# Performance work log

Hardware: AMD Instinct MI355X
Metric: run time of the kernel (lower is better)

## Reference

```python
import jax, jax.numpy as jnp
import numpy as np

B, T, E, H = 4, 4096, 1024, 64  # batch, seq_len, embed dim, head_size


def setup_inputs() -> dict:
    key = jax.random.key(0)
    kx, kk, kq, kv = jax.random.split(key, 4)
    x = jax.random.normal(kx, (B, T, E), dtype=jnp.float32)
    # nn.Linear(E, H, bias=False) weight, stored here as [E, H] (x @ W)
    Wk = jax.random.normal(kk, (E, H), dtype=jnp.float32) * 0.02
    Wq = jax.random.normal(kq, (E, H), dtype=jnp.float32) * 0.02
    Wv = jax.random.normal(kv, (E, H), dtype=jnp.float32) * 0.02
    return {"x": x, "Wk": Wk, "Wq": Wq, "Wv": Wv}


def reference(x, Wk, Wq, Wv):
    # single-head scaled dot-product attention (dropout p=0 -> identity)
    k = jnp.einsum("bte,eh->bth", x, Wk)
    q = jnp.einsum("bte,eh->bth", x, Wq)
    v = jnp.einsum("bte,eh->bth", x, Wv)
    scale = jnp.asarray(H, x.dtype) ** -0.5
    wei = jnp.einsum("bqh,bkh->bqk", q, k) * scale  # [B,T,T]
    wei = jax.nn.softmax(wei, axis=-1)
    out = jnp.einsum("bqk,bkh->bqh", wei, v)  # [B,T,H]
    return out
```

## Files before the change

kernel.cpp:

```cpp
#include <hip/hip_runtime.h>
#include <hip/hip_bf16.h>


typedef __attribute__((ext_vector_type(8))) short short8;
typedef __attribute__((ext_vector_type(4))) short short4v;
typedef __attribute__((ext_vector_type(4))) float f32x4;
typedef __attribute__((ext_vector_type(2))) unsigned uint2v;

#define LOG2E 1.44269504f

__device__ inline short f2bf(float f) {
  union { __hip_bfloat16 h; short s; } u; u.h = __float2bfloat16(f); return u.s;
}
__device__ inline unsigned cvt_pk_bf16(float lo, float hi) {
  unsigned r;
  asm("v_cvt_pk_bf16_f32 %0, %1, %2" : "=v"(r) : "v"(lo), "v"(hi));
  return r;
}
__device__ inline void gl_lds16(const short* g, short* l) {
  __builtin_amdgcn_global_load_lds(
      (const __attribute__((address_space(1))) void*)g,
      (__attribute__((address_space(3))) void*)l, 16, 0, 0);
}
__device__ inline float xsum4g(float x) {
  uint2v a = __builtin_amdgcn_permlane32_swap(__float_as_uint(x), __float_as_uint(x), false, false);
  float y = __uint_as_float(a[0]) + __uint_as_float(a[1]);
  uint2v b = __builtin_amdgcn_permlane16_swap(__float_as_uint(y), __float_as_uint(y), false, false);
  return __uint_as_float(b[0]) + __uint_as_float(b[1]);
}

__global__ __launch_bounds__(256) void wtrans_kernel(
    const float* __restrict__ Wk, const float* __restrict__ Wq, const float* __restrict__ Wv,
    short* __restrict__ wT)
{
  const int m3 = blockIdx.y;
  const float* W = (m3 == 0) ? Wk : (m3 == 1) ? Wq : Wv;
  const float sc = (m3 == 1) ? 0.125f * LOG2E : 1.0f;
  int idx = blockIdx.x * 256 + threadIdx.x;
  int k = idx >> 6;
  int n = idx & 63;
  wT[(size_t)m3 * 65536 + n * 1024 + k] = f2bf(W[idx] * sc);
}

__global__ __launch_bounds__(256) void proj_kernel(
    const float* __restrict__ x, const short* __restrict__ wT,
    short* __restrict__ kout, short* __restrict__ qout, short* __restrict__ vTout)
{
  const int m3 = blockIdx.y;
  __shared__ __align__(16) short xl[64][72];
  __shared__ __align__(16) short wl[64][64];

  const int tid  = threadIdx.x;
  const int w    = tid >> 6;
  const int lane = tid & 63;
  const int lr   = lane & 15;
  const int lg   = lane >> 4;
  const int rowbase = blockIdx.x * 64;
  const short* wb = wT + (size_t)m3 * 65536;

  f32x4 acc[4];
#pragma unroll
  for (int j = 0; j < 4; ++j) acc[j] = (f32x4){0.f, 0.f, 0.f, 0.f};

  const int xr = tid >> 4;
  const int xc = (tid & 15) << 2;

  float4 nx[4];
  short8 nw[2];
#pragma unroll
  for (int p = 0; p < 4; ++p)
    nx[p] = *reinterpret_cast<const float4*>(&x[(size_t)(rowbase + xr + p * 16) * 1024 + xc]);
#pragma unroll
  for (int p = 0; p < 2; ++p) {
    int c = p * 256 + tid;
    nw[p] = *reinterpret_cast<const short8*>(&wb[(size_t)(c >> 3) * 1024 + ((c & 7) << 3)]);
  }

  for (int t = 0; t < 16; ++t) {
    if (t > 0) __syncthreads();

#pragma unroll
    for (int p = 0; p < 4; ++p) {
      uint2v pk;
      pk[0] = cvt_pk_bf16(nx[p].x, nx[p].y);
      pk[1] = cvt_pk_bf16(nx[p].z, nx[p].w);
      *reinterpret_cast<uint2v*>(&xl[xr + p * 16][xc]) = pk;
    }
#pragma unroll
    for (int p = 0; p < 2; ++p) {
      int c = p * 256 + tid;
      int n = c >> 3;
      int kk = (c & 7) << 3;
      *reinterpret_cast<short8*>(&wl[n][kk ^ ((n & 7) << 3)]) = nw[p];
    }
    __syncthreads();

    if (t < 15) {
      const int kb = (t + 1) * 64;
#pragma unroll
      for (int p = 0; p < 4; ++p)
        nx[p] = *reinterpret_cast<const float4*>(
            &x[(size_t)(rowbase + xr + p * 16) * 1024 + kb + xc]);
#pragma unroll
      for (int p = 0; p < 2; ++p) {
        int c = p * 256 + tid;
        nw[p] = *reinterpret_cast<const short8*>(
            &wb[(size_t)(c >> 3) * 1024 + kb + ((c & 7) << 3)]);
      }
    }

#pragma unroll
    for (int ks = 0; ks < 2; ++ks) {
      short8 a = *reinterpret_cast<const short8*>(&xl[16 * w + lr][ks * 32 + lg * 8]);
#pragma unroll
      for (int ct = 0; ct < 4; ++ct) {
        short8 b = *reinterpret_cast<const short8*>(
            &wl[16 * ct + lr][(ks * 32 + lg * 8) ^ ((lr & 7) << 3)]);
        acc[ct] = __builtin_amdgcn_mfma_f32_16x16x32_bf16(a, b, acc[ct], 0, 0, 0);
      }
    }
  }

  if (m3 == 2) {
    const int bb   = rowbase >> 12;
    const int tloc = (rowbase & 4095) + 16 * w + 4 * lg;
#pragma unroll
    for (int ct = 0; ct < 4; ++ct) {
      uint2v pk;
      pk[0] = cvt_pk_bf16(acc[ct][0], acc[ct][1]);
      pk[1] = cvt_pk_bf16(acc[ct][2], acc[ct][3]);
      size_t vidx = (size_t)bb * 64 * 4096 + (size_t)(16 * ct + lr) * 4096 + tloc;
      *reinterpret_cast<uint2v*>(&vTout[vidx]) = pk;
    }
  } else {
    short* out = (m3 == 0) ? kout : qout;
#pragma unroll
    for (int ct = 0; ct < 4; ++ct)
#pragma unroll
      for (int j = 0; j < 4; ++j) {
        int grow = rowbase + 16 * w + 4 * lg + j;
        out[(size_t)grow * 64 + 16 * ct + lr] = f2bf(acc[ct][j]);
      }
  }
}

__device__ __forceinline__ void softmax_t(f32x4 s[4], float& l, short8 pf[2]) {
#pragma unroll
  for (int a = 0; a < 4; ++a)
#pragma unroll
    for (int j = 0; j < 4; ++j) s[a][j] = __builtin_amdgcn_exp2f(s[a][j]);
  float ps = ((s[0][0] + s[0][1]) + (s[0][2] + s[0][3]))
           + ((s[1][0] + s[1][1]) + (s[1][2] + s[1][3]))
           + ((s[2][0] + s[2][1]) + (s[2][2] + s[2][3]))
           + ((s[3][0] + s[3][1]) + (s[3][2] + s[3][3]));
  l += ps;

  unsigned u[4][2];
#pragma unroll
  for (int a = 0; a < 4; ++a) {
    u[a][0] = cvt_pk_bf16(s[a][0], s[a][1]);
    u[a][1] = cvt_pk_bf16(s[a][2], s[a][3]);
  }
  unsigned t[2][4];
#pragma unroll
  for (int k1 = 0; k1 < 2; ++k1)
#pragma unroll
    for (int jj = 0; jj < 2; ++jj) {
      uint2v A = __builtin_amdgcn_permlane32_swap(u[2 * k1][jj], u[2 * k1 + 1][jj], false, false);
      uint2v T = __builtin_amdgcn_permlane16_swap(A[0], A[1], false, false);
      t[k1][jj]     = T[0];
      t[k1][2 + jj] = T[1];
    }
#pragma unroll
  for (int ks = 0; ks < 2; ++ks) {
    union { unsigned u4[4]; short8 s8; } cv;
    cv.u4[0] = t[ks][0]; cv.u4[1] = t[ks][1]; cv.u4[2] = t[ks][2]; cv.u4[3] = t[ks][3];
    pf[ks] = cv.s8;
  }
}

__global__ __launch_bounds__(256, 4) void attn_split_kernel(
    const short* __restrict__ qm, const short* __restrict__ km, const short* __restrict__ vT,
    float* __restrict__ opart, float* __restrict__ lpart,
    int S, int chunkTiles)
{
  const int nwg = 128 * S;
  int bid = (int)blockIdx.x;
  bid = (bid & 7) * (nwg >> 3) + (bid >> 3);
  const int qidx  = bid / S;
  const int split = bid % S;
  const int b  = qidx >> 5;
  const int qt = qidx & 31;
  const int tid  = threadIdx.x;
  const int w    = tid >> 6;
  const int lane = tid & 63;
  const int lr   = lane & 15;
  const int lg   = lane >> 4;

  __shared__ __align__(16) short kl[2][4096];
  __shared__ __align__(16) short vl[2][4096];

  const short* qb    = qm + ((size_t)(b * 4096 + qt * 128 + w * 32)) * 64;
  const short* kbase = km + (size_t)b * 262144;
  const short* vbase = vT + (size_t)b * 262144;

  const int lrow = lane >> 3;
  const int scol = ((lane & 7) * 8) ^ (lrow * 8);
  const int swr  = (lr & 7) << 3;

  auto stage = [&](int buf, int kt) {
    const short* kp = kbase + (size_t)kt * 4096;
    gl_lds16(kp + (8 * w + lrow) * 64 + scol,       &kl[buf][w * 512]);
    gl_lds16(kp + (8 * (w + 4) + lrow) * 64 + scol, &kl[buf][(w + 4) * 512]);
    const short* vp = vbase + (size_t)kt * 64;
    gl_lds16(vp + (size_t)(8 * w + lrow) * 4096 + scol,       &vl[buf][w * 512]);
    gl_lds16(vp + (size_t)(8 * (w + 4) + lrow) * 4096 + scol, &vl[buf][(w + 4) * 512]);
  };

  short8 qf0[2], qf1[2];
#pragma unroll
  for (int ks = 0; ks < 2; ++ks) {
    qf0[ks] = *reinterpret_cast<const short8*>(&qb[lr * 64 + ks * 32 + lg * 8]);
    qf1[ks] = *reinterpret_cast<const short8*>(&qb[(16 + lr) * 64 + ks * 32 + lg * 8]);
  }

  float l0 = 0.f, l1 = 0.f;
  f32x4 o0[4], o1[4];
#pragma unroll
  for (int dt = 0; dt < 4; ++dt) {
    o0[dt] = (f32x4){0.f, 0.f, 0.f, 0.f};
    o1[dt] = (f32x4){0.f, 0.f, 0.f, 0.f};
  }

  const int kt0 = split * chunkTiles;
  stage(0, kt0);
  __syncthreads();

  for (int it = 0; it < chunkTiles; ++it) {
    const int  cur  = it & 1;
    const bool more = (it + 1) < chunkTiles;
    if (more) stage(cur ^ 1, kt0 + it + 1);

    const short* klc = kl[cur];
    const short* vlc = vl[cur];

    f32x4 s0[4], s1[4];
#pragma unroll
    for (int a = 0; a < 4; ++a) {
      s0[a] = (f32x4){0.f, 0.f, 0.f, 0.f};
      s1[a] = (f32x4){0.f, 0.f, 0.f, 0.f};
    }
    __builtin_amdgcn_s_setprio(1);
#pragma unroll
    for (int ks = 0; ks < 2; ++ks)
#pragma unroll
      for (int kt16 = 0; kt16 < 4; ++kt16) {
        short8 kf = *reinterpret_cast<const short8*>(
            &klc[(kt16 * 16 + lr) * 64 + ((ks * 32 + lg * 8) ^ swr)]);
        s0[kt16] = __builtin_amdgcn_mfma_f32_16x16x32_bf16(kf, qf0[ks], s0[kt16], 0, 0, 0);
        s1[kt16] = __builtin_amdgcn_mfma_f32_16x16x32_bf16(kf, qf1[ks], s1[kt16], 0, 0, 0);
      }
    __builtin_amdgcn_s_setprio(0);

    short8 pf0[2], pf1[2];
    softmax_t(s0, l0, pf0);
    softmax_t(s1, l1, pf1);

    __builtin_amdgcn_s_setprio(1);
#pragma unroll
    for (int ks = 0; ks < 2; ++ks)
#pragma unroll
      for (int dt = 0; dt < 4; ++dt) {
        short8 vf = *reinterpret_cast<const short8*>(
            &vlc[(dt * 16 + lr) * 64 + ((ks * 32 + lg * 8) ^ swr)]);
        o0[dt] = __builtin_amdgcn_mfma_f32_16x16x32_bf16(vf, pf0[ks], o0[dt], 0, 0, 0);
        o1[dt] = __builtin_amdgcn_mfma_f32_16x16x32_bf16(vf, pf1[ks], o1[dt], 0, 0, 0);
      }
    __builtin_amdgcn_s_setprio(0);

    if (more) __syncthreads();
  }

  l0 = xsum4g(l0);
  l1 = xsum4g(l1);
  const int rowg = b * 4096 + qt * 128 + w * 32 + lr;
  float* ob0 = opart + ((size_t)split * 16384 + rowg) * 64;
  float* ob1 = ob0 + 16 * 64;
#pragma unroll
  for (int dt = 0; dt < 4; ++dt) {
    *reinterpret_cast<f32x4*>(&ob0[16 * dt + 4 * lg]) = o0[dt];
    *reinterpret_cast<f32x4*>(&ob1[16 * dt + 4 * lg]) = o1[dt];
  }
  if (lane < 16) {
    lpart[split * 16384 + rowg]      = l0;
    lpart[split * 16384 + rowg + 16] = l1;
  }
}

__global__ __launch_bounds__(256) void merge_kernel(
    const float* __restrict__ opart, const float* __restrict__ lpart,
    float* __restrict__ out, int S)
{
  int gid = blockIdx.x * 256 + threadIdx.x;
  int row = gid >> 4;
  int c4  = (gid & 15) << 2;
  float denom = 0.f;
  float ax = 0.f, ay = 0.f, az = 0.f, aw = 0.f;
  for (int s = 0; s < S; ++s) {
    denom += lpart[s * 16384 + row];
    float4 op = *reinterpret_cast<const float4*>(&opart[((size_t)s * 16384 + row) * 64 + c4]);
    ax += op.x; ay += op.y; az += op.z; aw += op.w;
  }
  float inv = 1.f / denom;
  float4 r; r.x = ax * inv; r.y = ay * inv; r.z = az * inv; r.w = aw * inv;
  *reinterpret_cast<float4*>(&out[(size_t)row * 64 + c4]) = r;
}

extern "C" void kernel_launch(void* const* d_in, const int* in_sizes, int n_in,
                              void* d_out, int out_size, void* d_ws, size_t ws_size,
                              hipStream_t stream) {
  const float* x  = (const float*)d_in[0];
  const float* Wk = (const float*)d_in[1];
  const float* Wq = (const float*)d_in[2];
  const float* Wv = (const float*)d_in[3];

  const size_t MH = (size_t)16384 * 64;
  short* kmat = (short*)d_ws;
  short* qmat = kmat + MH;
  short* vTm  = qmat + MH;
  short* wT   = vTm + MH;

  dim3 gw(256, 3);
  wtrans_kernel<<<gw, 256, 0, stream>>>(Wk, Wq, Wv, wT);
  dim3 gproj(256, 3);
  proj_kernel<<<gproj, 256, 0, stream>>>(x, wT, kmat, qmat, vTm);

  const size_t head_bytes = (3 * MH + 196608) * sizeof(short);
  const size_t o_bytes    = MH * sizeof(float);
  const size_t l_bytes    = (size_t)16384 * sizeof(float);
  int S = 8;
  while (S > 1 && head_bytes + (size_t)S * (o_bytes + l_bytes) > ws_size) S >>= 1;

  float* opart = (float*)((char*)d_ws + head_bytes);
  float* lpart = opart + (size_t)S * MH;
  attn_split_kernel<<<128 * S, 256, 0, stream>>>(qmat, kmat, vTm,
                                                 opart, lpart, S, 64 / S);
  merge_kernel<<<1024, 256, 0, stream>>>(opart, lpart, (float*)d_out, S);
}
```

Before: 58.31 us.

## Software-pipeline PV MFMA of previous tile with QK of current tile

Splits K/V staging and triple-buffers V in LDS so that each iteration issues the P·V MFMAs for the previous tile interleaved with the Q·K MFMAs for the current tile. Softmax then runs after both matrix phases, and a final epilogue handles the last tile's P·V. The aim is to hide softmax latency behind MFMA work and give the scheduler more independent matrix instructions. In exchange it uses more LDS and registers (pf kept live across iterations), and the first iteration does a dummy P·V with zero P.

```diff
diff --git a/kernel.cpp b/kernel.cpp
--- a/kernel.cpp
+++ b/kernel.cpp
@@ -198,7 +198,7 @@
   const int lg   = lane >> 4;
 
   __shared__ __align__(16) short kl[2][4096];
-  __shared__ __align__(16) short vl[2][4096];
+  __shared__ __align__(16) short vl[3][4096];
 
   const short* qb    = qm + ((size_t)(b * 4096 + qt * 128 + w * 32)) * 64;
   const short* kbase = km + (size_t)b * 262144;
@@ -208,10 +208,12 @@
   const int scol = ((lane & 7) * 8) ^ (lrow * 8);
   const int swr  = (lr & 7) << 3;
 
-  auto stage = [&](int buf, int kt) {
+  auto stageK = [&](int buf, int kt) {
     const short* kp = kbase + (size_t)kt * 4096;
     gl_lds16(kp + (8 * w + lrow) * 64 + scol,       &kl[buf][w * 512]);
     gl_lds16(kp + (8 * (w + 4) + lrow) * 64 + scol, &kl[buf][(w + 4) * 512]);
+  };
+  auto stageV = [&](int buf, int kt) {
     const short* vp = vbase + (size_t)kt * 64;
     gl_lds16(vp + (size_t)(8 * w + lrow) * 4096 + scol,       &vl[buf][w * 512]);
     gl_lds16(vp + (size_t)(8 * (w + 4) + lrow) * 4096 + scol, &vl[buf][(w + 4) * 512]);
@@ -231,18 +233,23 @@
     o0[dt] = (f32x4){0.f, 0.f, 0.f, 0.f};
     o1[dt] = (f32x4){0.f, 0.f, 0.f, 0.f};
   }
+  short8 pf0[2] = {}, pf1[2] = {};
 
   const int kt0 = split * chunkTiles;
-  stage(0, kt0);
+  stageK(0, kt0);
+  stageV(0, kt0);
+  stageV(2, kt0);
   __syncthreads();
 
   for (int it = 0; it < chunkTiles; ++it) {
-    const int  cur  = it & 1;
     const bool more = (it + 1) < chunkTiles;
-    if (more) stage(cur ^ 1, kt0 + it + 1);
-
-    const short* klc = kl[cur];
-    const short* vlc = vl[cur];
+    if (more) {
+      stageK((it + 1) & 1, kt0 + it + 1);
+      stageV((it + 1) % 3, kt0 + it + 1);
+    }
+
+    const short* klc = kl[it & 1];
+    const short* vlp = vl[(it + 2) % 3];
 
     f32x4 s0[4], s1[4];
 #pragma unroll
@@ -250,9 +257,10 @@
       s0[a] = (f32x4){0.f, 0.f, 0.f, 0.f};
       s1[a] = (f32x4){0.f, 0.f, 0.f, 0.f};
     }
+
     __builtin_amdgcn_s_setprio(1);
 #pragma unroll
-    for (int ks = 0; ks < 2; ++ks)
+    for (int ks = 0; ks < 2; ++ks) {
 #pragma unroll
       for (int kt16 = 0; kt16 < 4; ++kt16) {
         short8 kf = *reinterpret_cast<const short8*>(
@@ -260,25 +268,33 @@
         s0[kt16] = __builtin_amdgcn_mfma_f32_16x16x32_bf16(kf, qf0[ks], s0[kt16], 0, 0, 0);
         s1[kt16] = __builtin_amdgcn_mfma_f32_16x16x32_bf16(kf, qf1[ks], s1[kt16], 0, 0, 0);
       }
+#pragma unroll
+      for (int dt = 0; dt < 4; ++dt) {
+        short8 vf = *reinterpret_cast<const short8*>(
+            &vlp[(dt * 16 + lr) * 64 + ((ks * 32 + lg * 8) ^ swr)]);
+        o0[dt] = __builtin_amdgcn_mfma_f32_16x16x32_bf16(vf, pf0[ks], o0[dt], 0, 0, 0);
+        o1[dt] = __builtin_amdgcn_mfma_f32_16x16x32_bf16(vf, pf1[ks], o1[dt], 0, 0, 0);
+      }
+    }
     __builtin_amdgcn_s_setprio(0);
 
-    short8 pf0[2], pf1[2];
     softmax_t(s0, l0, pf0);
     softmax_t(s1, l1, pf1);
 
-    __builtin_amdgcn_s_setprio(1);
+    if (more) __syncthreads();
+  }
+
+  {
+    const short* vll = vl[(chunkTiles - 1) % 3];
 #pragma unroll
     for (int ks = 0; ks < 2; ++ks)
 #pragma unroll
       for (int dt = 0; dt < 4; ++dt) {
         short8 vf = *reinterpret_cast<const short8*>(
-            &vlc[(dt * 16 + lr) * 64 + ((ks * 32 + lg * 8) ^ swr)]);
+            &vll[(dt * 16 + lr) * 64 + ((ks * 32 + lg * 8) ^ swr)]);
         o0[dt] = __builtin_amdgcn_mfma_f32_16x16x32_bf16(vf, pf0[ks], o0[dt], 0, 0, 0);
         o1[dt] = __builtin_amdgcn_mfma_f32_16x16x32_bf16(vf, pf1[ks], o1[dt], 0, 0, 0);
       }
-    __builtin_amdgcn_s_setprio(0);
-
-    if (more) __syncthreads();
   }
 
   l0 = xsum4g(l0);
```

Result: slower. 74.02 us (+26.9%).
